# Performance work log

Hardware: AMD Instinct MI355X
Metric: run time of the kernel (lower is better)

Reference implementation:

```python
import jax, jax.numpy as jnp
import numpy as np

B, S, E, H = 8, 2048, 1024, 64

def setup_inputs() -> dict:
    key = jax.random.key(0)
    ks = jax.random.split(key, 10)
    inp = {
        'input_Q': jax.random.normal(ks[0], (B, S, E), dtype=jnp.float32),
        'input_K': jax.random.normal(ks[1], (B, S, E), dtype=jnp.float32),
        'input_V': jax.random.normal(ks[2], (B, S, E), dtype=jnp.float32),
        'mask': jax.random.randint(ks[3], (B, S, S), 0, 2) > 0,
        # Linear params: torch Linear(E, H) -> weight [H, E], use as x @ W^T + b; store transposed [E, H]
        'Wq': jax.random.normal(ks[4], (E, H), dtype=jnp.float32) / np.sqrt(E),
        'bq': jnp.zeros((H,), dtype=jnp.float32),
        'Wk': jax.random.normal(ks[5], (E, H), dtype=jnp.float32) / np.sqrt(E),
        'bk': jnp.zeros((H,), dtype=jnp.float32),
        'Wv': jax.random.normal(ks[6], (E, H), dtype=jnp.float32) / np.sqrt(E),
        'bv': jnp.zeros((H,), dtype=jnp.float32),
    }
    return inp

def reference(input_Q, input_K, input_V, mask, Wq, bq, Wk, bk, Wv, bv):
    Q = jnp.einsum('bse,eh->bsh', input_Q, Wq) + bq  # [B,S,H]
    K = jnp.einsum('bse,eh->bsh', input_K, Wk) + bk
    V = jnp.einsum('bse,eh->bsh', input_V, Wv) + bv
    scores = jnp.einsum('bqh,bkh->bqk', Q, K) / np.sqrt(H).astype(np.float32)  # [B,S,S]
    # faithful to masked_fill_(mask, 1e-10) BEFORE softmax
    scores = jnp.where(mask, jnp.float32(1e-10), scores)
    attn = jax.nn.softmax(scores, axis=-1)
    # dropout is identity in eval/reference mode
    return jnp.einsum('bqk,bkh->bqh', attn, V)
```

## Files before the change

### kernel.cpp

```cpp
#include <hip/hip_runtime.h>
#include <hip/hip_bf16.h>
#include <stdint.h>

constexpr int Bc = 8, Sc = 2048, Ec = 1024, Hc = 64;

typedef __bf16 bf16x8 __attribute__((ext_vector_type(8)));
typedef float f32x4 __attribute__((ext_vector_type(4)));
typedef unsigned short ushort8 __attribute__((ext_vector_type(8)));

static __device__ __forceinline__ unsigned short f2bf(float f) {
  uint32_t u = __builtin_bit_cast(uint32_t, f);
  u = u + 0x7fffu + ((u >> 16) & 1u);
  return (unsigned short)(u >> 16);
}
static __device__ __forceinline__ bf16x8 ldb8(const unsigned short* p) {
  return __builtin_bit_cast(bf16x8, *(const ushort8*)p);
}

__global__ __launch_bounds__(256) void wt_kernel(
    const float* __restrict__ Wq, const float* __restrict__ Wk,
    const float* __restrict__ Wv, unsigned short* __restrict__ Wt) {
  int idx = blockIdx.x * 256 + threadIdx.x;
  int m = idx >> 16;
  int r = idx & 65535;
  int h = r >> 10;
  int e = r & 1023;
  const float* W = (m == 0) ? Wq : (m == 1) ? Wk : Wv;
  Wt[idx] = f2bf(W[e * Hc + h]);
}

__global__ __launch_bounds__(256) void proj_kernel(
    const float* __restrict__ Xq, const float* __restrict__ Xk,
    const float* __restrict__ Xv, const float* __restrict__ bq,
    const float* __restrict__ bk, const float* __restrict__ bv,
    const unsigned short* __restrict__ Wt,
    unsigned short* __restrict__ Qb, unsigned short* __restrict__ Kb,
    unsigned short* __restrict__ Vt) {
  const int mat = blockIdx.y;
  const float* X = (mat == 0) ? Xq : (mat == 1) ? Xk : Xv;
  const float* bias = (mat == 0) ? bq : (mat == 1) ? bk : bv;
  const unsigned short* W = Wt + mat * (Hc * Ec);

  const int tid = threadIdx.x;
  const int wave = tid >> 6, lane = tid & 63;
  const int row0 = blockIdx.x * 64;
  const int arow = row0 + wave * 16 + (lane & 15);
  const int kofs = (lane >> 4) * 8;

  const float* aptr = X + (size_t)arow * Ec + kofs;

  f32x4 acc[4];
  for (int nt = 0; nt < 4; nt++) acc[nt] = (f32x4){0.f, 0.f, 0.f, 0.f};

  const unsigned short* wbase = W + (size_t)(lane & 15) * Ec + kofs;

  for (int kb = 0; kb < Ec; kb += 32) {
    float4 a0 = *(const float4*)(aptr + kb);
    float4 a1 = *(const float4*)(aptr + kb + 4);
    ushort8 au;
    au[0] = f2bf(a0.x); au[1] = f2bf(a0.y); au[2] = f2bf(a0.z); au[3] = f2bf(a0.w);
    au[4] = f2bf(a1.x); au[5] = f2bf(a1.y); au[6] = f2bf(a1.z); au[7] = f2bf(a1.w);
    bf16x8 afrag = __builtin_bit_cast(bf16x8, au);
#pragma unroll
    for (int nt = 0; nt < 4; nt++) {
      bf16x8 bfrag = ldb8(wbase + (size_t)(nt * 16) * Ec + kb);
      acc[nt] = __builtin_amdgcn_mfma_f32_16x16x32_bf16(afrag, bfrag, acc[nt], 0, 0, 0);
    }
  }

  __shared__ unsigned short tile[64][72];
#pragma unroll
  for (int nt = 0; nt < 4; nt++) {
    float bv_ = bias[nt * 16 + (lane & 15)];
#pragma unroll
    for (int r = 0; r < 4; r++) {
      float v = acc[nt][r] + bv_;
      tile[wave * 16 + (lane >> 4) * 4 + r][nt * 16 + (lane & 15)] = f2bf(v);
    }
  }
  __syncthreads();

  if (mat < 2) {
    unsigned short* out = (mat == 0) ? Qb : Kb;
    int s_l = tid >> 2;
    int hs = (tid & 3) * 16;
    ushort8 v0 = *(const ushort8*)&tile[s_l][hs];
    ushort8 v1 = *(const ushort8*)&tile[s_l][hs + 8];
    unsigned short* dst = out + (size_t)(row0 + s_l) * Hc + hs;
    *(ushort8*)dst = v0;
    *(ushort8*)(dst + 8) = v1;
  } else {
    int h = tid >> 2;
    int ss = (tid & 3) * 16;
    int bb = row0 >> 11;
    int sbase = (row0 & 2047) + ss;
    ushort8 v0, v1;
#pragma unroll
    for (int i = 0; i < 8; i++) {
      v0[i] = tile[ss + i][h];
      v1[i] = tile[ss + 8 + i][h];
    }
    unsigned short* dst = Vt + ((size_t)bb * Hc + h) * Sc + sbase;
    *(ushort8*)dst = v0;
    *(ushort8*)(dst + 8) = v1;
  }
}

__global__ __launch_bounds__(256) void attn_kernel(
    const unsigned short* __restrict__ Qb, const unsigned short* __restrict__ Kb,
    const unsigned short* __restrict__ Vt, const int* __restrict__ mask,
    float* __restrict__ out) {
  const int b = blockIdx.y;
  const int q0 = blockIdx.x * 64;
  const int tid = threadIdx.x;
  const int wave = tid >> 6, lane = tid & 63;

  __shared__ unsigned short Ks[64][72];
  __shared__ unsigned short Vs[64][72];
  __shared__ unsigned short Ps[4][16][72];

  const int qrow = q0 + wave * 16 + (lane & 15);
  const unsigned short* qptr = Qb + ((size_t)b * Sc + qrow) * Hc + (lane >> 4) * 8;
  bf16x8 aQ0 = ldb8(qptr);
  bf16x8 aQ1 = ldb8(qptr + 32);

  const int qout_row = q0 + wave * 16 + (lane >> 4) * 4;
  float m_r[4], l_r[4];
  f32x4 Oacc[4];
#pragma unroll
  for (int r = 0; r < 4; r++) { m_r[r] = -INFINITY; l_r[r] = 0.f; }
#pragma unroll
  for (int ht = 0; ht < 4; ht++) Oacc[ht] = (f32x4){0.f, 0.f, 0.f, 0.f};

  const int* mbase[4];
#pragma unroll
  for (int r = 0; r < 4; r++)
    mbase[r] = mask + ((size_t)b * Sc + qout_row + r) * Sc + (lane & 15);

  for (int k0 = 0; k0 < Sc; k0 += 64) {
    __syncthreads();
    {
      int key = tid >> 2;
      int hs = (tid & 3) * 16;
      const unsigned short* kp = Kb + ((size_t)b * Sc + k0 + key) * Hc + hs;
      *(ushort8*)&Ks[key][hs] = *(const ushort8*)kp;
      *(ushort8*)&Ks[key][hs + 8] = *(const ushort8*)(kp + 8);
      const unsigned short* vp = Vt + ((size_t)b * Hc + key) * Sc + k0 + hs;
      *(ushort8*)&Vs[key][hs] = *(const ushort8*)vp;
      *(ushort8*)&Vs[key][hs + 8] = *(const ushort8*)(vp + 8);
    }
    __syncthreads();

    float sv[4][4];
#pragma unroll
    for (int nt = 0; nt < 4; nt++) {
      const unsigned short* kr = &Ks[nt * 16 + (lane & 15)][(lane >> 4) * 8];
      bf16x8 bK0 = ldb8(kr);
      bf16x8 bK1 = ldb8(kr + 32);
      f32x4 s = (f32x4){0.f, 0.f, 0.f, 0.f};
      s = __builtin_amdgcn_mfma_f32_16x16x32_bf16(aQ0, bK0, s, 0, 0, 0);
      s = __builtin_amdgcn_mfma_f32_16x16x32_bf16(aQ1, bK1, s, 0, 0, 0);
#pragma unroll
      for (int r = 0; r < 4; r++) {
        int mv = mbase[r][k0 + nt * 16];
        float x = s[r] * 0.125f;
        sv[nt][r] = mv ? 1e-10f : x;
      }
    }

    float rmax[4];
#pragma unroll
    for (int r = 0; r < 4; r++) {
      rmax[r] = fmaxf(fmaxf(sv[0][r], sv[1][r]), fmaxf(sv[2][r], sv[3][r]));
#pragma unroll
      for (int off = 1; off < 16; off <<= 1)
        rmax[r] = fmaxf(rmax[r], __shfl_xor(rmax[r], off, 64));
    }

    float alpha[4], p[4][4], psum[4];
#pragma unroll
    for (int r = 0; r < 4; r++) {
      float mnew = fmaxf(m_r[r], rmax[r]);
      alpha[r] = __expf(m_r[r] - mnew);
      m_r[r] = mnew;
      psum[r] = 0.f;
    }
#pragma unroll
    for (int nt = 0; nt < 4; nt++)
#pragma unroll
      for (int r = 0; r < 4; r++) {
        p[nt][r] = __expf(sv[nt][r] - m_r[r]);
        psum[r] += p[nt][r];
      }
#pragma unroll
    for (int r = 0; r < 4; r++) {
#pragma unroll
      for (int off = 1; off < 16; off <<= 1)
        psum[r] += __shfl_xor(psum[r], off, 64);
      l_r[r] = l_r[r] * alpha[r] + psum[r];
    }
#pragma unroll
    for (int ht = 0; ht < 4; ht++)
#pragma unroll
      for (int r = 0; r < 4; r++) Oacc[ht][r] *= alpha[r];

#pragma unroll
    for (int nt = 0; nt < 4; nt++)
#pragma unroll
      for (int r = 0; r < 4; r++)
        Ps[wave][(lane >> 4) * 4 + r][nt * 16 + (lane & 15)] = f2bf(p[nt][r]);
    __syncthreads();

#pragma unroll
    for (int ks = 0; ks < 2; ks++) {
      bf16x8 aP = ldb8(&Ps[wave][lane & 15][ks * 32 + (lane >> 4) * 8]);
#pragma unroll
      for (int ht = 0; ht < 4; ht++) {
        bf16x8 bV = ldb8(&Vs[ht * 16 + (lane & 15)][ks * 32 + (lane >> 4) * 8]);
        Oacc[ht] = __builtin_amdgcn_mfma_f32_16x16x32_bf16(aP, bV, Oacc[ht], 0, 0, 0);
      }
    }
  }

#pragma unroll
  for (int ht = 0; ht < 4; ht++)
#pragma unroll
    for (int r = 0; r < 4; r++)
      out[((size_t)b * Sc + qout_row + r) * Hc + ht * 16 + (lane & 15)] =
          Oacc[ht][r] / l_r[r];
}

extern "C" void kernel_launch(void* const* d_in, const int* in_sizes, int n_in,
                              void* d_out, int out_size, void* d_ws, size_t ws_size,
                              hipStream_t stream) {
  const float* Xq = (const float*)d_in[0];
  const float* Xk = (const float*)d_in[1];
  const float* Xv = (const float*)d_in[2];
  const int* mask = (const int*)d_in[3];
  const float* Wq = (const float*)d_in[4];
  const float* bq = (const float*)d_in[5];
  const float* Wk = (const float*)d_in[6];
  const float* bk = (const float*)d_in[7];
  const float* Wv = (const float*)d_in[8];
  const float* bv = (const float*)d_in[9];

  unsigned short* Qb = (unsigned short*)d_ws;
  unsigned short* Kb = Qb + (size_t)Bc * Sc * Hc;
  unsigned short* Vt = Kb + (size_t)Bc * Sc * Hc;
  unsigned short* Wt = Vt + (size_t)Bc * Sc * Hc;

  wt_kernel<<<dim3(3 * Hc * Ec / 256), 256, 0, stream>>>(Wq, Wk, Wv, Wt);
  proj_kernel<<<dim3(Bc * Sc / 64, 3), 256, 0, stream>>>(Xq, Xk, Xv, bq, bk, bv,
                                                         Wt, Qb, Kb, Vt);
  attn_kernel<<<dim3(Sc / 64, Bc), 256, 0, stream>>>(Qb, Kb, Vt, mask,
                                                     (float*)d_out);
}
```

Baseline: 403.4 us.

## Split attention keys across waves with cross-wave softmax merge; shrink projection tiles

The attention kernel now gives each block 16 query rows and splits the 2048 keys across its four waves, 512 keys each. K and V fragments are read straight from global memory instead of being staged in shared memory, and the partial max, sum and output are merged across waves through shared memory at the end. This removes per-tile __syncthreads, raises the grid size fourfold, and issues mask loads before the score MFMAs. The 1/sqrt(H) scale is folded into Wq and bq during weight conversion. The projection kernel moves to 16-row tiles with one output column tile per wave, which gives more blocks but reloads each X row for every wave and uses less K/V reuse.

```diff
diff --git a/kernel.cpp b/kernel.cpp
--- a/kernel.cpp
+++ b/kernel.cpp
@@ -7,6 +7,7 @@
 typedef __bf16 bf16x8 __attribute__((ext_vector_type(8)));
 typedef float f32x4 __attribute__((ext_vector_type(4)));
 typedef unsigned short ushort8 __attribute__((ext_vector_type(8)));
+typedef unsigned short ushort4v __attribute__((ext_vector_type(4)));
 
 static __device__ __forceinline__ unsigned short f2bf(float f) {
   uint32_t u = __builtin_bit_cast(uint32_t, f);
@@ -26,10 +27,11 @@
   int h = r >> 10;
   int e = r & 1023;
   const float* W = (m == 0) ? Wq : (m == 1) ? Wk : Wv;
-  Wt[idx] = f2bf(W[e * Hc + h]);
-}
-
-__global__ __launch_bounds__(256) void proj_kernel(
+  float scale = (m == 0) ? 0.125f : 1.0f;
+  Wt[idx] = f2bf(W[e * Hc + h] * scale);
+}
+
+__global__ __launch_bounds__(256, 8) void proj_kernel(
     const float* __restrict__ Xq, const float* __restrict__ Xk,
     const float* __restrict__ Xv, const float* __restrict__ bq,
     const float* __restrict__ bk, const float* __restrict__ bv,
@@ -39,92 +41,77 @@
   const int mat = blockIdx.y;
   const float* X = (mat == 0) ? Xq : (mat == 1) ? Xk : Xv;
   const float* bias = (mat == 0) ? bq : (mat == 1) ? bk : bv;
+  const float bscale = (mat == 0) ? 0.125f : 1.0f;
   const unsigned short* W = Wt + mat * (Hc * Ec);
 
   const int tid = threadIdx.x;
   const int wave = tid >> 6, lane = tid & 63;
-  const int row0 = blockIdx.x * 64;
-  const int arow = row0 + wave * 16 + (lane & 15);
+  const int row0 = blockIdx.x * 16;
+  const int arow = row0 + (lane & 15);
   const int kofs = (lane >> 4) * 8;
 
   const float* aptr = X + (size_t)arow * Ec + kofs;
-
-  f32x4 acc[4];
-  for (int nt = 0; nt < 4; nt++) acc[nt] = (f32x4){0.f, 0.f, 0.f, 0.f};
-
-  const unsigned short* wbase = W + (size_t)(lane & 15) * Ec + kofs;
+  const unsigned short* wbase =
+      W + (size_t)(wave * 16 + (lane & 15)) * Ec + kofs;
+
+  f32x4 acc = (f32x4){0.f, 0.f, 0.f, 0.f};
 
   for (int kb = 0; kb < Ec; kb += 32) {
     float4 a0 = *(const float4*)(aptr + kb);
     float4 a1 = *(const float4*)(aptr + kb + 4);
+    bf16x8 bfrag = ldb8(wbase + kb);
     ushort8 au;
     au[0] = f2bf(a0.x); au[1] = f2bf(a0.y); au[2] = f2bf(a0.z); au[3] = f2bf(a0.w);
     au[4] = f2bf(a1.x); au[5] = f2bf(a1.y); au[6] = f2bf(a1.z); au[7] = f2bf(a1.w);
     bf16x8 afrag = __builtin_bit_cast(bf16x8, au);
-#pragma unroll
-    for (int nt = 0; nt < 4; nt++) {
-      bf16x8 bfrag = ldb8(wbase + (size_t)(nt * 16) * Ec + kb);
-      acc[nt] = __builtin_amdgcn_mfma_f32_16x16x32_bf16(afrag, bfrag, acc[nt], 0, 0, 0);
-    }
-  }
-
-  __shared__ unsigned short tile[64][72];
-#pragma unroll
-  for (int nt = 0; nt < 4; nt++) {
-    float bv_ = bias[nt * 16 + (lane & 15)];
-#pragma unroll
-    for (int r = 0; r < 4; r++) {
-      float v = acc[nt][r] + bv_;
-      tile[wave * 16 + (lane >> 4) * 4 + r][nt * 16 + (lane & 15)] = f2bf(v);
-    }
+    acc = __builtin_amdgcn_mfma_f32_16x16x32_bf16(afrag, bfrag, acc, 0, 0, 0);
+  }
+
+  __shared__ unsigned short tile[16][72];
+  {
+    float bcol = bias[wave * 16 + (lane & 15)] * bscale;
+#pragma unroll
+    for (int r = 0; r < 4; r++)
+      tile[(lane >> 4) * 4 + r][wave * 16 + (lane & 15)] = f2bf(acc[r] + bcol);
   }
   __syncthreads();
 
   if (mat < 2) {
     unsigned short* out = (mat == 0) ? Qb : Kb;
-    int s_l = tid >> 2;
-    int hs = (tid & 3) * 16;
-    ushort8 v0 = *(const ushort8*)&tile[s_l][hs];
-    ushort8 v1 = *(const ushort8*)&tile[s_l][hs + 8];
-    unsigned short* dst = out + (size_t)(row0 + s_l) * Hc + hs;
-    *(ushort8*)dst = v0;
-    *(ushort8*)(dst + 8) = v1;
+    int s_l = tid >> 4;
+    int c0 = (tid & 15) * 4;
+    ushort4v v = *(const ushort4v*)&tile[s_l][c0];
+    *(ushort4v*)(out + (size_t)(row0 + s_l) * Hc + c0) = v;
   } else {
     int h = tid >> 2;
-    int ss = (tid & 3) * 16;
+    int sc = (tid & 3) * 4;
     int bb = row0 >> 11;
-    int sbase = (row0 & 2047) + ss;
-    ushort8 v0, v1;
-#pragma unroll
-    for (int i = 0; i < 8; i++) {
-      v0[i] = tile[ss + i][h];
-      v1[i] = tile[ss + 8 + i][h];
-    }
-    unsigned short* dst = Vt + ((size_t)bb * Hc + h) * Sc + sbase;
-    *(ushort8*)dst = v0;
-    *(ushort8*)(dst + 8) = v1;
-  }
-}
-
-__global__ __launch_bounds__(256) void attn_kernel(
+    int sbase = (row0 & 2047) + sc;
+    ushort4v v;
+#pragma unroll
+    for (int i = 0; i < 4; i++) v[i] = tile[sc + i][h];
+    *(ushort4v*)(Vt + ((size_t)bb * Hc + h) * Sc + sbase) = v;
+  }
+}
+
+__global__ __launch_bounds__(256, 4) void attn_kernel(
     const unsigned short* __restrict__ Qb, const unsigned short* __restrict__ Kb,
     const unsigned short* __restrict__ Vt, const int* __restrict__ mask,
     float* __restrict__ out) {
   const int b = blockIdx.y;
-  const int q0 = blockIdx.x * 64;
+  const int q0 = blockIdx.x * 16;
   const int tid = threadIdx.x;
   const int wave = tid >> 6, lane = tid & 63;
 
-  __shared__ unsigned short Ks[64][72];
-  __shared__ unsigned short Vs[64][72];
   __shared__ unsigned short Ps[4][16][72];
-
-  const int qrow = q0 + wave * 16 + (lane & 15);
-  const unsigned short* qptr = Qb + ((size_t)b * Sc + qrow) * Hc + (lane >> 4) * 8;
+  __shared__ float sm[4][16], sl[4][16];
+  __shared__ float Os[4][16][64];
+
+  const unsigned short* qptr =
+      Qb + ((size_t)b * Sc + q0 + (lane & 15)) * Hc + (lane >> 4) * 8;
   bf16x8 aQ0 = ldb8(qptr);
   bf16x8 aQ1 = ldb8(qptr + 32);
 
-  const int qout_row = q0 + wave * 16 + (lane >> 4) * 4;
   float m_r[4], l_r[4];
   f32x4 Oacc[4];
 #pragma unroll
@@ -132,40 +119,38 @@
 #pragma unroll
   for (int ht = 0; ht < 4; ht++) Oacc[ht] = (f32x4){0.f, 0.f, 0.f, 0.f};
 
-  const int* mbase[4];
+  const int* mrow[4];
 #pragma unroll
   for (int r = 0; r < 4; r++)
-    mbase[r] = mask + ((size_t)b * Sc + qout_row + r) * Sc + (lane & 15);
-
-  for (int k0 = 0; k0 < Sc; k0 += 64) {
-    __syncthreads();
-    {
-      int key = tid >> 2;
-      int hs = (tid & 3) * 16;
-      const unsigned short* kp = Kb + ((size_t)b * Sc + k0 + key) * Hc + hs;
-      *(ushort8*)&Ks[key][hs] = *(const ushort8*)kp;
-      *(ushort8*)&Ks[key][hs + 8] = *(const ushort8*)(kp + 8);
-      const unsigned short* vp = Vt + ((size_t)b * Hc + key) * Sc + k0 + hs;
-      *(ushort8*)&Vs[key][hs] = *(const ushort8*)vp;
-      *(ushort8*)&Vs[key][hs + 8] = *(const ushort8*)(vp + 8);
-    }
-    __syncthreads();
+    mrow[r] = mask + ((size_t)b * Sc + q0 + (lane >> 4) * 4 + r) * Sc + (lane & 15);
+
+  const unsigned short* kbase =
+      Kb + ((size_t)b * Sc) * Hc + (size_t)(lane & 15) * Hc + (lane >> 4) * 8;
+  const unsigned short* vbase[4];
+#pragma unroll
+  for (int ht = 0; ht < 4; ht++)
+    vbase[ht] = Vt + ((size_t)b * Hc + ht * 16 + (lane & 15)) * Sc + (lane >> 4) * 8;
+
+  for (int c = 0; c < 8; c++) {
+    const int koff = wave * 512 + c * 64;
+
+    int mv[4][4];
+#pragma unroll
+    for (int nt = 0; nt < 4; nt++)
+#pragma unroll
+      for (int r = 0; r < 4; r++) mv[nt][r] = mrow[r][koff + nt * 16];
 
     float sv[4][4];
 #pragma unroll
     for (int nt = 0; nt < 4; nt++) {
-      const unsigned short* kr = &Ks[nt * 16 + (lane & 15)][(lane >> 4) * 8];
-      bf16x8 bK0 = ldb8(kr);
-      bf16x8 bK1 = ldb8(kr + 32);
+      const unsigned short* kp = kbase + (size_t)(koff + nt * 16) * Hc;
+      bf16x8 bK0 = ldb8(kp);
+      bf16x8 bK1 = ldb8(kp + 32);
       f32x4 s = (f32x4){0.f, 0.f, 0.f, 0.f};
       s = __builtin_amdgcn_mfma_f32_16x16x32_bf16(aQ0, bK0, s, 0, 0, 0);
       s = __builtin_amdgcn_mfma_f32_16x16x32_bf16(aQ1, bK1, s, 0, 0, 0);
 #pragma unroll
-      for (int r = 0; r < 4; r++) {
-        int mv = mbase[r][k0 + nt * 16];
-        float x = s[r] * 0.125f;
-        sv[nt][r] = mv ? 1e-10f : x;
-      }
+      for (int r = 0; r < 4; r++) sv[nt][r] = mv[nt][r] ? 1e-10f : s[r];
     }
 
     float rmax[4];
@@ -209,25 +194,55 @@
 #pragma unroll
       for (int r = 0; r < 4; r++)
         Ps[wave][(lane >> 4) * 4 + r][nt * 16 + (lane & 15)] = f2bf(p[nt][r]);
-    __syncthreads();
 
 #pragma unroll
     for (int ks = 0; ks < 2; ks++) {
       bf16x8 aP = ldb8(&Ps[wave][lane & 15][ks * 32 + (lane >> 4) * 8]);
 #pragma unroll
       for (int ht = 0; ht < 4; ht++) {
-        bf16x8 bV = ldb8(&Vs[ht * 16 + (lane & 15)][ks * 32 + (lane >> 4) * 8]);
+        bf16x8 bV = ldb8(vbase[ht] + koff + ks * 32);
         Oacc[ht] = __builtin_amdgcn_mfma_f32_16x16x32_bf16(aP, bV, Oacc[ht], 0, 0, 0);
       }
     }
   }
 
+  if ((lane & 15) == 0) {
+#pragma unroll
+    for (int r = 0; r < 4; r++) {
+      sm[wave][(lane >> 4) * 4 + r] = m_r[r];
+      sl[wave][(lane >> 4) * 4 + r] = l_r[r];
+    }
+  }
+  __syncthreads();
+
+  float coef[4];
+#pragma unroll
+  for (int r = 0; r < 4; r++) {
+    int row = (lane >> 4) * 4 + r;
+    float M = fmaxf(fmaxf(sm[0][row], sm[1][row]), fmaxf(sm[2][row], sm[3][row]));
+    coef[r] = __expf(m_r[r] - M);
+  }
 #pragma unroll
   for (int ht = 0; ht < 4; ht++)
 #pragma unroll
     for (int r = 0; r < 4; r++)
-      out[((size_t)b * Sc + qout_row + r) * Hc + ht * 16 + (lane & 15)] =
-          Oacc[ht][r] / l_r[r];
+      Os[wave][(lane >> 4) * 4 + r][ht * 16 + (lane & 15)] = Oacc[ht][r] * coef[r];
+  __syncthreads();
+
+  {
+#pragma unroll
+    for (int i = 0; i < 4; i++) {
+      int row = wave * 4 + i;
+      float M = fmaxf(fmaxf(sm[0][row], sm[1][row]), fmaxf(sm[2][row], sm[3][row]));
+      float L = sl[0][row] * __expf(sm[0][row] - M) +
+                sl[1][row] * __expf(sm[1][row] - M) +
+                sl[2][row] * __expf(sm[2][row] - M) +
+                sl[3][row] * __expf(sm[3][row] - M);
+      float acc = Os[0][row][lane] + Os[1][row][lane] +
+                  Os[2][row][lane] + Os[3][row][lane];
+      out[((size_t)b * Sc + q0 + row) * Hc + lane] = acc / L;
+    }
+  }
 }
 
 extern "C" void kernel_launch(void* const* d_in, const int* in_sizes, int n_in,
@@ -250,8 +265,8 @@
   unsigned short* Wt = Vt + (size_t)Bc * Sc * Hc;
 
   wt_kernel<<<dim3(3 * Hc * Ec / 256), 256, 0, stream>>>(Wq, Wk, Wv, Wt);
-  proj_kernel<<<dim3(Bc * Sc / 64, 3), 256, 0, stream>>>(Xq, Xk, Xv, bq, bk, bv,
+  proj_kernel<<<dim3(Bc * Sc / 16, 3), 256, 0, stream>>>(Xq, Xk, Xv, bq, bk, bv,
                                                          Wt, Qb, Kb, Vt);
-  attn_kernel<<<dim3(Sc / 64, Bc), 256, 0, stream>>>(Qb, Kb, Vt, mask,
+  attn_kernel<<<dim3(Sc / 16, Bc), 256, 0, stream>>>(Qb, Kb, Vt, mask,
                                                      (float*)d_out);
 }
```

Result: slower. 441.0 us (+9.3%).
